# Performance work log

Hardware: AMD Instinct MI355X
Metric: run time of the kernel (lower is better)

The kernel has to match this reference:

```python
import jax, jax.numpy as jnp
import numpy as np

N_NODES = 50000
N_EDGES = 1600000
IN_FEATS = 128
ENC_H = 20
DEC_H = 64


def setup_inputs() -> dict:
    key = jax.random.key(0)
    ks = jax.random.split(key, 14)
    inp = {}
    inp["x"] = jax.random.normal(ks[0], (N_NODES, IN_FEATS), dtype=jnp.float32)
    inp["edge_index"] = jax.random.randint(ks[1], (2, N_EDGES), 0, N_NODES, dtype=jnp.int64)
    inp["node_id"] = 0
    inp["noise_normal"] = jax.random.normal(ks[2], (N_EDGES, ENC_H), dtype=jnp.float32)
    inp["noise_u"] = jax.random.uniform(ks[3], (N_EDGES, 1), dtype=jnp.float32)
    # parameters (glorot-ish init)
    def lin(k, fan_in, fan_out):
        s = 1.0 / np.sqrt(fan_in)
        return jax.random.uniform(k, (fan_in, fan_out), jnp.float32, -s, s)
    inp["W_gc"] = lin(ks[4], IN_FEATS, ENC_H)
    inp["b_gc"] = jnp.zeros((ENC_H,), jnp.float32)
    inp["W_mu"] = lin(ks[5], 3 * ENC_H, ENC_H)
    inp["b_mu"] = jnp.zeros((ENC_H,), jnp.float32)
    inp["W_var"] = lin(ks[6], 3 * ENC_H, ENC_H)
    inp["b_var"] = jnp.zeros((ENC_H,), jnp.float32)
    inp["W_d1"] = lin(ks[7], ENC_H, DEC_H)
    inp["b_d1"] = jnp.zeros((DEC_H,), jnp.float32)
    inp["W_d2"] = lin(ks[8], DEC_H, 1)
    inp["b_d2"] = jnp.zeros((1,), jnp.float32)
    return inp


def _gcn_conv(x, edge_index, W, b):
    """PyG-style GCNConv: add self-loops, symmetric D^-1/2 (A+I) D^-1/2 norm."""
    n = x.shape[0]
    sl = jnp.arange(n, dtype=edge_index.dtype)
    row = jnp.concatenate([edge_index[0], sl])  # source
    col = jnp.concatenate([edge_index[1], sl])  # target
    xw = x @ W  # [N, H]
    deg = jax.ops.segment_sum(jnp.ones_like(col, dtype=xw.dtype), col, num_segments=n)
    dinv = jnp.where(deg > 0, jax.lax.rsqrt(deg), 0.0)
    norm = dinv[row] * dinv[col]  # [E+N]
    out = jax.ops.segment_sum(xw[row] * norm[:, None], col, num_segments=n)
    return out + b


def reference(x, edge_index, node_id, noise_normal, noise_u,
              W_gc, b_gc, W_mu, b_mu, W_var, b_var, W_d1, b_d1, W_d2, b_d2):
    # GCN encoder
    x1 = jax.nn.relu(_gcn_conv(x, edge_index, W_gc, b_gc))  # [N, H]
    # per-edge concat: [src_embed | dst_embed | node_id_embed]
    rows, cols = edge_index[0], edge_index[1]
    node_embed = jnp.broadcast_to(x1[node_id][None, :], (rows.shape[0], x1.shape[1]))
    x2 = jnp.concatenate([x1[rows], x1[cols], node_embed], axis=1)  # [E, 3H]
    # variational heads + reparameterization
    mu = x2 @ W_mu + b_mu
    sigma = jnp.exp(x2 @ W_var + b_var)
    z = mu + sigma * noise_normal  # [E, H]
    # decoder MLP
    h = jax.nn.relu(z @ W_d1 + b_d1)
    sampling_weights = jax.nn.relu(h @ W_d2 + b_d2)  # [E, 1]
    # gumbel-sigmoid sample (training=True, bias=0.0 -> bias'=1e-4, temperature=1.0)
    bias = 0.0001
    eps = (bias - (1.0 - bias)) * noise_u + (1.0 - bias)
    gate = jnp.log(eps) - jnp.log(1.0 - eps) + sampling_weights
    return jax.nn.sigmoid(gate)
```

## Files before the change

kernel.cpp:

```cpp
#include <hip/hip_runtime.h>

#define NFEAT 128
#define H 20
#define DH 64
#define SCAN_T 1024
#define BE2 128
#define NB 192
#define HW 12800

typedef __attribute__((ext_vector_type(8))) short short8;
typedef __attribute__((ext_vector_type(4))) float f32x4;

__device__ __forceinline__ unsigned short f2bf(float f) {
    union { float f; unsigned u; } v; v.f = f;
    unsigned r = v.u + 0x7fff + ((v.u >> 16) & 1);
    return (unsigned short)(r >> 16);
}
__device__ __forceinline__ unsigned pk2(unsigned short a, unsigned short b) {
    return (unsigned)a | ((unsigned)b << 16);
}
__device__ __forceinline__ float bfel(uint4 v, int j) {
    unsigned word = (j < 2) ? v.x : (j < 4) ? v.y : (j < 6) ? v.z : v.w;
    unsigned u = (j & 1) ? (word & 0xFFFF0000u) : (word << 16);
    return __int_as_float((int)u);
}

template <int CTRL>
__device__ __forceinline__ float dpp_add(float x) {
    int y = __builtin_amdgcn_update_dpp(0, __float_as_int(x), CTRL, 0xF, 0xF, true);
    return x + __int_as_float(y);
}
__device__ __forceinline__ float sum16(float x) {
    x = dpp_add<0xB1>(x);
    x = dpp_add<0x4E>(x);
    x = dpp_add<0x124>(x);
    x = dpp_add<0x128>(x);
    return x;
}

__global__ __launch_bounds__(256) void k_prep(const float* __restrict__ Wd1,
                                              unsigned short* __restrict__ Bd1,
                                              int* __restrict__ deg, int* __restrict__ csum,
                                              float* __restrict__ bcat2, int N) {
    int t = blockIdx.x * blockDim.x + threadIdx.x;
    if (t < N) deg[t] = 0;
    if (t < 256) csum[t] = 0;
    if (t < 128) bcat2[t] = 0.f;
    if (t < 256) {
        int f = t >> 6, l = t & 63;
        int n = f * 16 + (l & 15);
#pragma unroll
        for (int j = 0; j < 8; j++) {
            int k = (l >> 4) * 8 + j;
            float v = (k < H) ? Wd1[k * DH + n] : 0.f;
            Bd1[(size_t)f * 512 + l * 8 + j] = f2bf(v);
        }
    }
}

__global__ __launch_bounds__(512) void k_hist(const int* __restrict__ cols,
                                              unsigned* __restrict__ hist, int* __restrict__ csum,
                                              unsigned char* __restrict__ rank,
                                              int E, int N) {
    __shared__ unsigned h[HW];
    __shared__ int cs[256];
    int wstride = (N + 3) >> 2;
    int nchunks = (N + 255) >> 8;
    for (int i = threadIdx.x; i < wstride; i += 512) h[i] = 0;
    if (threadIdx.x < 256) cs[threadIdx.x] = 0;
    __syncthreads();
    int chunk = (E + NB - 1) / NB;
    int beg = blockIdx.x * chunk, end = min(beg + chunk, E);
    for (int i = beg + threadIdx.x; i < end; i += 512) {
        int c = __builtin_nontemporal_load(cols + i);
        int sh = (c & 3) * 8;
        unsigned old = atomicAdd(&h[c >> 2], 1u << sh);
        rank[i] = (unsigned char)((old >> sh) & 0xFF);
    }
    __syncthreads();
    unsigned* dst = hist + (size_t)blockIdx.x * wstride;
    for (int i = threadIdx.x; i < wstride; i += 512) {
        unsigned w = h[i];
        dst[i] = w;
        if (w) {
            int s = (w & 0xFF) + ((w >> 8) & 0xFF) + ((w >> 16) & 0xFF) + (w >> 24);
            atomicAdd(&cs[i >> 6], s);
        }
    }
    __syncthreads();
    for (int j = threadIdx.x; j < nchunks; j += 512)
        if (cs[j]) atomicAdd(&csum[j], cs[j]);
}

__global__ __launch_bounds__(256) void k_scansmall(const int* __restrict__ chunkSum,
                                                   int* __restrict__ chunkOff, int nb) {
    __shared__ int sc[256];
    int t = threadIdx.x;
    int v0 = (t < nb) ? chunkSum[t] : 0;
    sc[t] = v0;
    __syncthreads();
    for (int off = 1; off < 256; off <<= 1) {
        int v = (t >= off) ? sc[t - off] : 0;
        __syncthreads();
        sc[t] += v;
        __syncthreads();
    }
    if (t < nb) chunkOff[t] = sc[t] - v0;
}

__global__ __launch_bounds__(256) void k_bases(const unsigned* __restrict__ hist,
                                               const int* __restrict__ chunkOff,
                                               unsigned char* __restrict__ delta,
                                               int* __restrict__ offsets, int* __restrict__ deg,
                                               int N, int E) {
    __shared__ int sc[256];
    int c = blockIdx.x * 256 + threadIdx.x;
    int wstride = (N + 3) >> 2;
    int sh = (c & 3) * 8;
    bool valid = c < N;
    int cw = valid ? (c >> 2) : 0;
    unsigned cnt[NB / 4];
    int d = 0;
#pragma unroll
    for (int b = 0; b < NB; b++) {
        unsigned w = hist[(size_t)b * wstride + cw];
        unsigned byte = (w >> sh) & 0xFF;
        if ((b & 3) == 0) cnt[b >> 2] = byte;
        else cnt[b >> 2] |= byte << ((b & 3) * 8);
        d += (int)byte;
    }
    if (!valid) d = 0;
    sc[threadIdx.x] = d;
    __syncthreads();
    for (int off = 1; off < 256; off <<= 1) {
        int v = (threadIdx.x >= off) ? sc[threadIdx.x - off] : 0;
        __syncthreads();
        sc[threadIdx.x] += v;
        __syncthreads();
    }
    if (valid) {
        int base = chunkOff[blockIdx.x] + sc[threadIdx.x] - d;
        offsets[c] = base;
        deg[c] = d;
        int run = 0;
#pragma unroll
        for (int b = 0; b < NB; b++) {
            delta[(size_t)b * N + c] = (unsigned char)run;
            run += (int)((cnt[b >> 2] >> ((b & 3) * 8)) & 0xFF);
        }
    }
    if (blockIdx.x == 0 && threadIdx.x == 0) offsets[N] = E;
}

__global__ __launch_bounds__(256) void k_place(const int* __restrict__ rows, const int* __restrict__ cols,
                                               const int* __restrict__ offsets,
                                               const unsigned char* __restrict__ delta,
                                               const unsigned char* __restrict__ rank,
                                               unsigned short* __restrict__ srcs, int E, int N, int chunk) {
    int e = blockIdx.x * 256 + threadIdx.x;
    if (e >= E) return;
    int c = cols[e];
    int r = rows[e];
    int b = e / chunk;
    int pos = offsets[c] + (int)delta[(size_t)b * N + c] + (int)rank[e];
    srcs[pos] = (unsigned short)r;
}

__global__ __launch_bounds__(256) void k_deg(const int* __restrict__ cols, int* __restrict__ deg, int E) {
    int t = blockIdx.x * blockDim.x + threadIdx.x;
    if (t < E) atomicAdd(&deg[cols[t]], 1);
}

__global__ __launch_bounds__(SCAN_T) void k_scan(const int* __restrict__ deg, int* __restrict__ offsets,
                                                 int* __restrict__ cursor, int N) {
    __shared__ int sums[SCAN_T];
    int t = threadIdx.x;
    int chunk = (N + SCAN_T - 1) / SCAN_T;
    int beg = t * chunk;
    int end = min(beg + chunk, N);
    int s = 0;
    for (int i = beg; i < end; i++) s += deg[i];
    sums[t] = s;
    __syncthreads();
    for (int off = 1; off < SCAN_T; off <<= 1) {
        int v = (t >= off) ? sums[t - off] : 0;
        __syncthreads();
        sums[t] += v;
        __syncthreads();
    }
    int run = (t == 0) ? 0 : sums[t - 1];
    for (int i = beg; i < end; i++) {
        offsets[i] = run;
        cursor[i] = run;
        run += deg[i];
    }
    if (t == SCAN_T - 1) offsets[N] = sums[SCAN_T - 1];
}

__global__ __launch_bounds__(256) void k_bucket_csr(const int* __restrict__ rows, const int* __restrict__ cols,
                                                    int* __restrict__ cursor, int* __restrict__ srcs, int E) {
    int e = blockIdx.x * blockDim.x + threadIdx.x;
    if (e >= E) return;
    int pos = atomicAdd(&cursor[cols[e]], 1);
    srcs[pos] = rows[e];
}

__global__ __launch_bounds__(256) void k_xw_xs(const float* __restrict__ x, const float* __restrict__ Wgc,
                                               const int* __restrict__ deg,
                                               float* __restrict__ xs, int N) {
    __shared__ float Ws[NFEAT * H];
    for (int i = threadIdx.x; i < NFEAT * H; i += blockDim.x) Ws[i] = Wgc[i];
    __syncthreads();
    int n = blockIdx.x * blockDim.x + threadIdx.x;
    if (n >= N) return;
    float acc[H];
#pragma unroll
    for (int j = 0; j < H; j++) acc[j] = 0.f;
    const float4* x4 = (const float4*)(x + (size_t)n * NFEAT);
#pragma unroll 4
    for (int k4 = 0; k4 < NFEAT / 4; k4++) {
        float4 xv = x4[k4];
#pragma unroll
        for (int s = 0; s < 4; s++) {
            float xk = (s == 0) ? xv.x : (s == 1) ? xv.y : (s == 2) ? xv.z : xv.w;
            const float4* wrow = (const float4*)(Ws + (k4 * 4 + s) * H);
#pragma unroll
            for (int q = 0; q < 5; q++) {
                float4 w = wrow[q];
                acc[q * 4 + 0] += xk * w.x;
                acc[q * 4 + 1] += xk * w.y;
                acc[q * 4 + 2] += xk * w.z;
                acc[q * 4 + 3] += xk * w.w;
            }
        }
    }
    float di = rsqrtf((float)(deg[n] + 1));
    float4* o = (float4*)(xs + (size_t)n * H);
#pragma unroll
    for (int q = 0; q < 5; q++)
        o[q] = make_float4(acc[q * 4 + 0] * di, acc[q * 4 + 1] * di, acc[q * 4 + 2] * di, acc[q * 4 + 3] * di);
}

template <typename IT>
__device__ __forceinline__ void gather_core16(const float* __restrict__ xs, const IT* __restrict__ idx,
                                              int beg, int end, int n, int sl, int degn,
                                              const float* __restrict__ bgc,
                                              unsigned short* __restrict__ PAo, unsigned short* __restrict__ PBo,
                                              int nid, const float* __restrict__ Wmu, const float* __restrict__ Wvar,
                                              const float* __restrict__ bmu, const float* __restrict__ bvar,
                                              float* __restrict__ bcat2) {
    float acc[H];
    if (sl == 0) {
        const float4* self = (const float4*)(xs + (size_t)n * H);
#pragma unroll
        for (int q = 0; q < 5; q++) {
            float4 v = self[q];
            acc[q * 4 + 0] = v.x; acc[q * 4 + 1] = v.y; acc[q * 4 + 2] = v.z; acc[q * 4 + 3] = v.w;
        }
    } else {
#pragma unroll
        for (int j = 0; j < H; j++) acc[j] = 0.f;
    }
#pragma unroll 2
    for (int i = beg + sl; i < end; i += 16) {
        int r = (int)__builtin_nontemporal_load(idx + i);
        const float4* p = (const float4*)(xs + (size_t)r * H);
#pragma unroll
        for (int q = 0; q < 5; q++) {
            float4 v = p[q];
            acc[q * 4 + 0] += v.x; acc[q * 4 + 1] += v.y; acc[q * 4 + 2] += v.z; acc[q * 4 + 3] += v.w;
        }
    }
#pragma unroll
    for (int j = 0; j < H; j++) acc[j] = sum16(acc[j]);
    float di = rsqrtf((float)(degn + 1));
    float x1f[H];
#pragma unroll
    for (int j = 0; j < H; j++) x1f[j] = fmaxf(di * acc[j] + bgc[j], 0.f);

#pragma unroll
    for (int t = 0; t < 5; t++) {
        int v = sl + 16 * t;
        int part = v / 20;
        int j = v - part * 20;
        const float* W = (part & 1) ? Wvar : Wmu;
        int k0 = (part < 2) ? 0 : 20;
        float s = 0.f;
#pragma unroll
        for (int k = 0; k < H; k++) s += x1f[k] * W[(k0 + k) * H + j];
        unsigned short* T = (part < 2) ? PAo : PBo;
        int off = (j < 16) ? ((j >> 3) * 16 + (part & 1) * 8 + (j & 7))
                           : (32 + (part & 1) * 4 + (j - 16));
        T[(size_t)n * 40 + off] = f2bf(s);
    }

    if (n == nid) {
#pragma unroll
        for (int base = 0; base < 48; base += 16) {
            int jj = base + sl;
            if (jj < 40) {
                bool ismu = jj < 20;
                int col = ismu ? jj : jj - 20;
                const float* W = ismu ? Wmu : Wvar;
                float s = ismu ? bmu[col] : bvar[col];
#pragma unroll
                for (int k = 0; k < H; k++) s += x1f[k] * W[(2 * H + k) * H + col];
                bcat2[ismu ? col : 64 + col] = s;
            }
        }
    }
}

__global__ __launch_bounds__(256) void k_gather_csr16(const float* __restrict__ xs, const unsigned short* __restrict__ srcs,
                                                      const int* __restrict__ offsets, const int* __restrict__ deg,
                                                      const float* __restrict__ bgc,
                                                      unsigned short* __restrict__ PAo, unsigned short* __restrict__ PBo,
                                                      const int* __restrict__ node_id,
                                                      const float* __restrict__ Wmu, const float* __restrict__ Wvar,
                                                      const float* __restrict__ bmu, const float* __restrict__ bvar,
                                                      float* __restrict__ bcat2, int N) {
    int wave = (blockIdx.x * 256 + threadIdx.x) >> 6;
    int lane = threadIdx.x & 63;
    int n = wave * 4 + (lane >> 4);
    if (n >= N) return;
    gather_core16(xs, srcs, offsets[n], offsets[n + 1], n, lane & 15, deg[n], bgc, PAo, PBo,
                  node_id[0], Wmu, Wvar, bmu, bvar, bcat2);
}

__global__ __launch_bounds__(256) void k_gather_csr(const float* __restrict__ xs, const int* __restrict__ srcs,
                                                    const int* __restrict__ offsets, const int* __restrict__ deg,
                                                    const float* __restrict__ bgc,
                                                    unsigned short* __restrict__ PAo, unsigned short* __restrict__ PBo,
                                                    const int* __restrict__ node_id,
                                                    const float* __restrict__ Wmu, const float* __restrict__ Wvar,
                                                    const float* __restrict__ bmu, const float* __restrict__ bvar,
                                                    float* __restrict__ bcat2, int N) {
    int wave = (blockIdx.x * 256 + threadIdx.x) >> 6;
    int lane = threadIdx.x & 63;
    int n = wave * 4 + (lane >> 4);
    if (n >= N) return;
    gather_core16(xs, srcs, offsets[n], offsets[n + 1], n, lane & 15, deg[n], bgc, PAo, PBo,
                  node_id[0], Wmu, Wvar, bmu, bvar, bcat2);
}

__device__ __forceinline__ short8 build_a2(const unsigned short* __restrict__ PA,
                                           const unsigned short* __restrict__ PBt,
                                           const float* __restrict__ noise_n,
                                           int em, int r, int c, int q,
                                           const float (&bm)[8], const float (&bv)[8]) {
    uint4 pam = {0, 0, 0, 0}, pav = pam, pbm = pam, pbv = pam;
    float nz[8];
#pragma unroll
    for (int j = 0; j < 8; j++) nz[j] = 0.f;
    if (q < 2) {
        const char* pa = (const char*)PA + (size_t)r * 80 + q * 32;
        const char* pb = (const char*)PBt + (size_t)c * 80 + q * 32;
        pam = *(const uint4*)pa;  pav = *(const uint4*)(pa + 16);
        pbm = *(const uint4*)pb;  pbv = *(const uint4*)(pb + 16);
        const float* np = noise_n + (size_t)em * H + q * 8;
        float4 n0 = *(const float4*)np;
        float4 n1 = *(const float4*)(np + 4);
        nz[0] = n0.x; nz[1] = n0.y; nz[2] = n0.z; nz[3] = n0.w;
        nz[4] = n1.x; nz[5] = n1.y; nz[6] = n1.z; nz[7] = n1.w;
    } else if (q == 2) {
        const char* pa = (const char*)PA + (size_t)r * 80 + 64;
        const char* pb = (const char*)PBt + (size_t)c * 80 + 64;
        uint2 am = *(const uint2*)pa;
        uint2 av = *(const uint2*)(pa + 8);
        uint2 bm2 = *(const uint2*)pb;
        uint2 bv2 = *(const uint2*)(pb + 8);
        pam.x = am.x; pam.y = am.y;
        pav.x = av.x; pav.y = av.y;
        pbm.x = bm2.x; pbm.y = bm2.y;
        pbv.x = bv2.x; pbv.y = bv2.y;
        float4 n0 = *(const float4*)(noise_n + (size_t)em * H + 16);
        nz[0] = n0.x; nz[1] = n0.y; nz[2] = n0.z; nz[3] = n0.w;
    }
    unsigned zp[4];
#pragma unroll
    for (int jj = 0; jj < 4; jj++) {
        unsigned short zh[2];
#pragma unroll
        for (int h2 = 0; h2 < 2; h2++) {
            int j = jj * 2 + h2;
            float zmu = bfel(pam, j) + bfel(pbm, j) + bm[j];
            float zva = bfel(pav, j) + bfel(pbv, j) + bv[j];
            float z = zmu + __expf(zva) * nz[j];
            z = (q * 8 + j < 20) ? z : 0.f;
            zh[h2] = f2bf(z);
        }
        zp[jj] = pk2(zh[0], zh[1]);
    }
    union { unsigned u[4]; short8 s; } au;
    au.u[0] = zp[0]; au.u[1] = zp[1]; au.u[2] = zp[2]; au.u[3] = zp[3];
    return au.s;
}

__global__ __launch_bounds__(256) void k_mlp(
    const unsigned short* __restrict__ PA, const unsigned short* __restrict__ PBt,
    const int* __restrict__ rows, const int* __restrict__ cols,
    const float* __restrict__ noise_n, const float* __restrict__ noise_u,
    const unsigned short* __restrict__ Bd1g,
    const float* __restrict__ bcat2, const float* __restrict__ b_d1,
    const float* __restrict__ W_d2, const float* __restrict__ b_d2,
    float* __restrict__ out, int E) {

    int tid = threadIdx.x;
    int e0 = blockIdx.x * BE2;
    int l = tid & 63, w = tid >> 6;
    int m = l & 15, q = l >> 4;

    float bm[8], bv[8];
#pragma unroll
    for (int j = 0; j < 8; j++) { bm[j] = 0.f; bv[j] = 0.f; }
    if (q < 3) {
        float4 b0 = *(const float4*)(bcat2 + q * 8);
        float4 b1 = *(const float4*)(bcat2 + q * 8 + 4);
        bm[0] = b0.x; bm[1] = b0.y; bm[2] = b0.z; bm[3] = b0.w;
        bm[4] = b1.x; bm[5] = b1.y; bm[6] = b1.z; bm[7] = b1.w;
        float4 v0 = *(const float4*)(bcat2 + 64 + q * 8);
        float4 v1 = *(const float4*)(bcat2 + 64 + q * 8 + 4);
        bv[0] = v0.x; bv[1] = v0.y; bv[2] = v0.z; bv[3] = v0.w;
        bv[4] = v1.x; bv[5] = v1.y; bv[6] = v1.z; bv[7] = v1.w;
    }

    int ea0 = e0 + w * 16 + m;
    int ea1 = ea0 + 64;
    int em0 = (ea0 < E) ? ea0 : E - 1;
    int em1 = (ea1 < E) ? ea1 : E - 1;
    int r0 = rows[em0], c0 = cols[em0];
    int r1 = rows[em1], c1 = cols[em1];

    short8 a2_0 = (q < 3) ? build_a2(PA, PBt, noise_n, em0, r0, c0, q, bm, bv)
                          : short8{0, 0, 0, 0, 0, 0, 0, 0};
    short8 a2_1 = (q < 3) ? build_a2(PA, PBt, noise_n, em1, r1, c1, q, bm, bv)
                          : short8{0, 0, 0, 0, 0, 0, 0, 0};

    float p0a = 0.f, p1a = 0.f, p2a = 0.f, p3a = 0.f;
    float p0b = 0.f, p1b = 0.f, p2b = 0.f, p3b = 0.f;
#pragma unroll
    for (int t4 = 0; t4 < 4; t4++) {
        short8 bb = *(const short8*)(Bd1g + t4 * 512 + l * 8);
        f32x4 za = {0.f, 0.f, 0.f, 0.f};
        f32x4 zb = {0.f, 0.f, 0.f, 0.f};
        za = __builtin_amdgcn_mfma_f32_16x16x32_bf16(a2_0, bb, za, 0, 0, 0);
        zb = __builtin_amdgcn_mfma_f32_16x16x32_bf16(a2_1, bb, zb, 0, 0, 0);
        int col = t4 * 16 + m;
        float bias = b_d1[col], wo = W_d2[col];
        p0a += fmaxf(za[0] + bias, 0.f) * wo;
        p1a += fmaxf(za[1] + bias, 0.f) * wo;
        p2a += fmaxf(za[2] + bias, 0.f) * wo;
        p3a += fmaxf(za[3] + bias, 0.f) * wo;
        p0b += fmaxf(zb[0] + bias, 0.f) * wo;
        p1b += fmaxf(zb[1] + bias, 0.f) * wo;
        p2b += fmaxf(zb[2] + bias, 0.f) * wo;
        p3b += fmaxf(zb[3] + bias, 0.f) * wo;
    }
    p0a = sum16(p0a); p1a = sum16(p1a); p2a = sum16(p2a); p3a = sum16(p3a);
    p0b = sum16(p0b); p1b = sum16(p1b); p2b = sum16(p2b); p3b = sum16(p3b);
    if (m < 4) {
        float swa = (m == 0) ? p0a : (m == 1) ? p1a : (m == 2) ? p2a : p3a;
        float swb = (m == 0) ? p0b : (m == 1) ? p1b : (m == 2) ? p2b : p3b;
        int eA = e0 + w * 16 + q * 4 + m;
        int eB = eA + 64;
        if (eA < E) {
            float sw = fmaxf(swa + b_d2[0], 0.f);
            float u = noise_u[eA];
            float ev = 0.9999f - 0.9998f * u;
            out[eA] = ev / (ev + (1.f - ev) * __expf(-sw));
        }
        if (eB < E) {
            float sw = fmaxf(swb + b_d2[0], 0.f);
            float u = noise_u[eB];
            float ev = 0.9999f - 0.9998f * u;
            out[eB] = ev / (ev + (1.f - ev) * __expf(-sw));
        }
    }
}

extern "C" void kernel_launch(void* const* d_in, const int* in_sizes, int n_in,
                              void* d_out, int out_size, void* d_ws, size_t ws_size,
                              hipStream_t stream) {
    const int N = in_sizes[0] / NFEAT;
    const int E = in_sizes[1] / 2;

    const float* x       = (const float*)d_in[0];
    const int*   ei      = (const int*)d_in[1];
    const int*   rows    = ei;
    const int*   cols    = ei + E;
    const int*   node_id = (const int*)d_in[2];
    const float* noise_n = (const float*)d_in[3];
    const float* noise_u = (const float*)d_in[4];
    const float* Wgc  = (const float*)d_in[5];
    const float* bgc  = (const float*)d_in[6];
    const float* Wmu  = (const float*)d_in[7];
    const float* bmu  = (const float*)d_in[8];
    const float* Wvar = (const float*)d_in[9];
    const float* bvar = (const float*)d_in[10];
    const float* Wd1  = (const float*)d_in[11];
    const float* bd1  = (const float*)d_in[12];
    const float* Wd2  = (const float*)d_in[13];
    const float* bd2  = (const float*)d_in[14];
    float* out = (float*)d_out;

    const int B = 256;
    int gN  = (N + B - 1) / B;
    int gG  = (N + 15) / 16;
    int gE  = (E + B - 1) / B;
    int gM  = (E + BE2 - 1) / BE2;
    int nBins = (N + 255) / 256;
    int chunk = (E + NB - 1) / NB;

    char* ws = (char*)d_ws;
    size_t wstride   = (size_t)((N + 3) >> 2);
    size_t pa_sz     = (((size_t)N * 80) + 255) & ~255ULL;
    size_t hist_sz   = ((NB * wstride * 4) + 255) & ~255ULL;
    size_t histreg   = (hist_sz > 2 * pa_sz) ? hist_sz : 2 * pa_sz;
    size_t o_deg     = 0;
    size_t o_off     = o_deg  + (((size_t)N * 4 + 255) & ~255ULL);
    size_t o_csum    = o_off  + (((size_t)(N + 1) * 4 + 255) & ~255ULL);
    size_t o_coff    = o_csum + 1024;
    size_t o_hist    = o_coff + 1024;
    size_t o_delta   = o_hist  + histreg;
    size_t o_rank    = o_delta + (((size_t)NB * N + 255) & ~255ULL);
    size_t o_srcs    = o_rank  + (((size_t)E + 255) & ~255ULL);
    size_t o_xs      = o_srcs  + (((size_t)E * 2 + 255) & ~255ULL);
    size_t o_Bd1     = o_xs    + (((size_t)N * H * 4 + 255) & ~255ULL);
    size_t o_bcat2   = o_Bd1   + 4096;
    size_t need      = o_bcat2 + 512;

    bool main_path = (ws_size >= need) && (N <= 4 * HW) && (N < 65536) && (nBins <= 256);

    if (main_path) {
        int*   deg     = (int*)(ws + o_deg);
        int*   offsets = (int*)(ws + o_off);
        int*   csum    = (int*)(ws + o_csum);
        int*   coff    = (int*)(ws + o_coff);
        unsigned* hist = (unsigned*)(ws + o_hist);
        unsigned short* PA = (unsigned short*)(ws + o_hist);
        unsigned short* PB = (unsigned short*)(ws + o_hist + pa_sz);
        unsigned char* delta = (unsigned char*)(ws + o_delta);
        unsigned char* rank  = (unsigned char*)(ws + o_rank);
        unsigned short* srcs = (unsigned short*)(ws + o_srcs);
        float* xs      = (float*)(ws + o_xs);
        unsigned short* Bd1  = (unsigned short*)(ws + o_Bd1);
        float* bcat2   = (float*)(ws + o_bcat2);

        k_prep<<<gN, B, 0, stream>>>(Wd1, Bd1, deg, csum, bcat2, N);
        k_hist<<<NB, 512, 0, stream>>>(cols, hist, csum, rank, E, N);
        k_scansmall<<<1, B, 0, stream>>>(csum, coff, nBins);
        k_bases<<<nBins, B, 0, stream>>>(hist, coff, delta, offsets, deg, N, E);
        k_xw_xs<<<gN, B, 0, stream>>>(x, Wgc, deg, xs, N);
        k_place<<<gE, B, 0, stream>>>(rows, cols, offsets, delta, rank, srcs, E, N, chunk);
        k_gather_csr16<<<gG, B, 0, stream>>>(xs, srcs, offsets, deg, bgc, PA, PB,
                                             node_id, Wmu, Wvar, bmu, bvar, bcat2, N);
        k_mlp<<<gM, B, 0, stream>>>(PA, PB, rows, cols, noise_n, noise_u,
                                    Bd1, bcat2, bd1, Wd2, bd2, out, E);
    } else {
        size_t f_deg   = 0;
        size_t f_off   = f_deg + (((size_t)N * 4 + 255) & ~255ULL);
        size_t f_cur   = f_off + (((size_t)(N + 1) * 4 + 255) & ~255ULL);
        size_t f_srcs  = f_cur + (((size_t)N * 4 + 255) & ~255ULL);
        size_t f_xs    = f_srcs + (((size_t)E * 4 + 255) & ~255ULL);
        size_t f_PA    = f_xs + (((size_t)N * H * 4 + 255) & ~255ULL);
        size_t f_PB    = f_PA + pa_sz;
        size_t f_Bd1   = f_PB + pa_sz;
        size_t f_bcat2 = f_Bd1 + 4096;

        int*   deg     = (int*)(ws + f_deg);
        int*   offsets = (int*)(ws + f_off);
        int*   cursor  = (int*)(ws + f_cur);
        int*   srcs    = (int*)(ws + f_srcs);
        float* xs      = (float*)(ws + f_xs);
        unsigned short* PA = (unsigned short*)(ws + f_PA);
        unsigned short* PB = (unsigned short*)(ws + f_PB);
        unsigned short* Bd1 = (unsigned short*)(ws + f_Bd1);
        float* bcat2   = (float*)(ws + f_bcat2);

        k_prep<<<gN, B, 0, stream>>>(Wd1, Bd1, deg, cursor, bcat2, N);
        k_deg<<<gE, B, 0, stream>>>(cols, deg, E);
        k_scan<<<1, SCAN_T, 0, stream>>>(deg, offsets, cursor, N);
        k_bucket_csr<<<gE, B, 0, stream>>>(rows, cols, cursor, srcs, E);
        k_xw_xs<<<gN, B, 0, stream>>>(x, Wgc, deg, xs, N);
        k_gather_csr<<<gG, B, 0, stream>>>(xs, srcs, offsets, deg, bgc, PA, PB,
                                           node_id, Wmu, Wvar, bmu, bvar, bcat2, N);
        k_mlp<<<gM, B, 0, stream>>>(PA, PB, rows, cols, noise_n, noise_u,
                                    Bd1, bcat2, bd1, Wd2, bd2, out, E);
    }
}
```

Before: 443.8 us.

## Stage histogram tile in LDS for k_bases; halve edges per k_mlp block

```diff
diff --git a/kernel.cpp b/kernel.cpp
--- a/kernel.cpp
+++ b/kernel.cpp
@@ -4,7 +4,7 @@
 #define H 20
 #define DH 64
 #define SCAN_T 1024
-#define BE2 128
+#define BE 64
 #define NB 192
 #define HW 12800
 
@@ -113,17 +113,25 @@
                                                unsigned char* __restrict__ delta,
                                                int* __restrict__ offsets, int* __restrict__ deg,
                                                int N, int E) {
+    __shared__ unsigned hw[NB * 64];
     __shared__ int sc[256];
+    int wstride = (N + 3) >> 2;
+    int w0 = blockIdx.x * 64;
+    for (int i = threadIdx.x; i < NB * 64; i += 256) {
+        int b = i >> 6, wl = i & 63;
+        int gw = w0 + wl;
+        hw[i] = (gw < wstride) ? hist[(size_t)b * wstride + gw] : 0u;
+    }
+    __syncthreads();
     int c = blockIdx.x * 256 + threadIdx.x;
-    int wstride = (N + 3) >> 2;
     int sh = (c & 3) * 8;
     bool valid = c < N;
-    int cw = valid ? (c >> 2) : 0;
+    int wl = threadIdx.x >> 2;
     unsigned cnt[NB / 4];
     int d = 0;
 #pragma unroll
     for (int b = 0; b < NB; b++) {
-        unsigned w = hist[(size_t)b * wstride + cw];
+        unsigned w = hw[b * 64 + wl];
         unsigned byte = (w >> sh) & 0xFF;
         if ((b & 3) == 0) cnt[b >> 2] = byte;
         else cnt[b >> 2] |= byte << ((b & 3) * 8);
@@ -406,7 +414,7 @@
     float* __restrict__ out, int E) {
 
     int tid = threadIdx.x;
-    int e0 = blockIdx.x * BE2;
+    int e0 = blockIdx.x * BE;
     int l = tid & 63, w = tid >> 6;
     int m = l & 15, q = l >> 4;
 
@@ -424,56 +432,36 @@
         bv[4] = v1.x; bv[5] = v1.y; bv[6] = v1.z; bv[7] = v1.w;
     }
 
-    int ea0 = e0 + w * 16 + m;
-    int ea1 = ea0 + 64;
-    int em0 = (ea0 < E) ? ea0 : E - 1;
-    int em1 = (ea1 < E) ? ea1 : E - 1;
-    int r0 = rows[em0], c0 = cols[em0];
-    int r1 = rows[em1], c1 = cols[em1];
-
-    short8 a2_0 = (q < 3) ? build_a2(PA, PBt, noise_n, em0, r0, c0, q, bm, bv)
-                          : short8{0, 0, 0, 0, 0, 0, 0, 0};
-    short8 a2_1 = (q < 3) ? build_a2(PA, PBt, noise_n, em1, r1, c1, q, bm, bv)
-                          : short8{0, 0, 0, 0, 0, 0, 0, 0};
-
-    float p0a = 0.f, p1a = 0.f, p2a = 0.f, p3a = 0.f;
-    float p0b = 0.f, p1b = 0.f, p2b = 0.f, p3b = 0.f;
+    int ea = e0 + w * 16 + m;
+    int em = (ea < E) ? ea : E - 1;
+    int r = rows[em], c = cols[em];
+
+    short8 a2 = (q < 3) ? build_a2(PA, PBt, noise_n, em, r, c, q, bm, bv)
+                        : short8{0, 0, 0, 0, 0, 0, 0, 0};
+
+    float p0 = 0.f, p1 = 0.f, p2 = 0.f, p3 = 0.f;
 #pragma unroll
     for (int t4 = 0; t4 < 4; t4++) {
+        f32x4 acc = {0.f, 0.f, 0.f, 0.f};
         short8 bb = *(const short8*)(Bd1g + t4 * 512 + l * 8);
-        f32x4 za = {0.f, 0.f, 0.f, 0.f};
-        f32x4 zb = {0.f, 0.f, 0.f, 0.f};
-        za = __builtin_amdgcn_mfma_f32_16x16x32_bf16(a2_0, bb, za, 0, 0, 0);
-        zb = __builtin_amdgcn_mfma_f32_16x16x32_bf16(a2_1, bb, zb, 0, 0, 0);
+        acc = __builtin_amdgcn_mfma_f32_16x16x32_bf16(a2, bb, acc, 0, 0, 0);
         int col = t4 * 16 + m;
         float bias = b_d1[col], wo = W_d2[col];
-        p0a += fmaxf(za[0] + bias, 0.f) * wo;
-        p1a += fmaxf(za[1] + bias, 0.f) * wo;
-        p2a += fmaxf(za[2] + bias, 0.f) * wo;
-        p3a += fmaxf(za[3] + bias, 0.f) * wo;
-        p0b += fmaxf(zb[0] + bias, 0.f) * wo;
-        p1b += fmaxf(zb[1] + bias, 0.f) * wo;
-        p2b += fmaxf(zb[2] + bias, 0.f) * wo;
-        p3b += fmaxf(zb[3] + bias, 0.f) * wo;
-    }
-    p0a = sum16(p0a); p1a = sum16(p1a); p2a = sum16(p2a); p3a = sum16(p3a);
-    p0b = sum16(p0b); p1b = sum16(p1b); p2b = sum16(p2b); p3b = sum16(p3b);
+        p0 += fmaxf(acc[0] + bias, 0.f) * wo;
+        p1 += fmaxf(acc[1] + bias, 0.f) * wo;
+        p2 += fmaxf(acc[2] + bias, 0.f) * wo;
+        p3 += fmaxf(acc[3] + bias, 0.f) * wo;
+    }
+    p0 = sum16(p0); p1 = sum16(p1); p2 = sum16(p2); p3 = sum16(p3);
     if (m < 4) {
-        float swa = (m == 0) ? p0a : (m == 1) ? p1a : (m == 2) ? p2a : p3a;
-        float swb = (m == 0) ? p0b : (m == 1) ? p1b : (m == 2) ? p2b : p3b;
-        int eA = e0 + w * 16 + q * 4 + m;
-        int eB = eA + 64;
-        if (eA < E) {
-            float sw = fmaxf(swa + b_d2[0], 0.f);
-            float u = noise_u[eA];
+        float swv = (m == 0) ? p0 : (m == 1) ? p1 : (m == 2) ? p2 : p3;
+        int e = e0 + w * 16 + q * 4 + m;
+        if (e < E) {
+            float sw = fmaxf(swv + b_d2[0], 0.f);
+            float u = noise_u[e];
             float ev = 0.9999f - 0.9998f * u;
-            out[eA] = ev / (ev + (1.f - ev) * __expf(-sw));
-        }
-        if (eB < E) {
-            float sw = fmaxf(swb + b_d2[0], 0.f);
-            float u = noise_u[eB];
-            float ev = 0.9999f - 0.9998f * u;
-            out[eB] = ev / (ev + (1.f - ev) * __expf(-sw));
+            float t = __expf(-sw);
+            out[e] = ev / (ev + (1.f - ev) * t);
         }
     }
 }
@@ -507,7 +495,7 @@
     int gN  = (N + B - 1) / B;
     int gG  = (N + 15) / 16;
     int gE  = (E + B - 1) / B;
-    int gM  = (E + BE2 - 1) / BE2;
+    int gM  = (E + BE - 1) / BE;
     int nBins = (N + 255) / 256;
     int chunk = (E + NB - 1) / NB;
 
```

Result: slower. 464.2 us (+4.6%).
